# Optimization experiments

Measured on AMD Instinct MI355X. Metric: run time of the kernel, lower is better.

Reference implementation:

```python
import jax, jax.numpy as jnp
import numpy as np
from jax import lax

IMG = 28
K = 3
OUT = IMG - K + 1  # 26

def setup_inputs() -> dict:
    key = jax.random.key(0)
    k1, k2, k3 = jax.random.split(key, 3)
    B = 32768
    x = jax.random.normal(k1, (B, IMG * IMG), dtype=jnp.float32)
    conv_w = jax.random.normal(k2, (K, K), dtype=jnp.float32)
    W = jax.random.normal(k3, (IMG * IMG - 0, 1), dtype=jnp.float32)  # placeholder
    W = jax.random.normal(k3, (OUT * OUT, 10), dtype=jnp.float32) * 0.02
    b = jnp.zeros((10,), dtype=jnp.float32)
    return {"x": x, "conv_w": conv_w, "W": W, "b": b}

def reference(x, conv_w, W, b):
    B = x.shape[0]
    img = x.reshape(B, 1, IMG, IMG)            # NCHW
    ker = conv_w.reshape(1, 1, K, K)           # OIHW
    # The original Convolve is cross-correlation (slice * weight), which
    # matches lax.conv_general_dilated's default semantics.
    conv = lax.conv_general_dilated(
        img, ker, window_strides=(1, 1), padding='VALID',
        dimension_numbers=('NCHW', 'OIHW', 'NCHW'))  # [B,1,26,26]
    h = jax.nn.relu(conv.reshape(B, OUT * OUT))
    return h @ W + b
```

## Files before the change

kernel.cpp:

```cpp
#include <hip/hip_runtime.h>

#define IMGD 28
#define OUTD 26
#define NCLS 10
#define NIMG 64
#define UPB 29
#define BWORDS (NIMG * UPB * 4)
#define NBAND 7
#define THREADS 1024
#define LDSTRIDE 11

typedef float v2f __attribute__((ext_vector_type(2)));

__device__ __forceinline__ void gload_lds16(const float* gp, float* lp) {
    __builtin_amdgcn_global_load_lds(
        (const __attribute__((address_space(1))) void*)gp,
        (__attribute__((address_space(3))) void*)lp, 16, 0, 0);
}

__device__ __forceinline__ void stage_band(const float* __restrict__ x,
                                           int img_base, int B, int r0,
                                           float* buf, int wv, int lane)
{
#pragma unroll
    for (int it = 0; it < 2; ++it) {
        const int fw = it * 16 + wv;
        if (fw < UPB) {
            const int f = fw * 64 + lane;
            const int g = f / UPB;
            const int s = f - g * UPB;
            const int q = (s == 28) ? 27 : s;
            int gi = img_base + g; if (gi >= B) gi = B - 1;
            const float* gp = x + (size_t)gi * (IMGD * IMGD) + r0 * IMGD + q * 4;
            gload_lds16(gp, buf + fw * 256);
        }
    }
}

template<int NU>
__device__ __forceinline__ void read_row(const float* buf, int lane, int br, int u0,
                                         float* dst)
{
    const float4* b4 = (const float4*)buf;
#pragma unroll
    for (int u = 0; u < NU; ++u) {
        float4 a = b4[lane * UPB + br * 7 + u0 + u];
        dst[4*u+0] = a.x; dst[4*u+1] = a.y; dst[4*u+2] = a.z; dst[4*u+3] = a.w;
    }
}

template<int WID, int OFF>
__device__ __forceinline__ void conv_row(const float* X, const float* Y, const float* Z,
                                         const float (&kk)[9],
                                         const float* __restrict__ wr, v2f* acc)
{
#pragma unroll
    for (int c = 0; c < WID; ++c) {
        float p0 = fmaf(X[OFF+c], kk[0], X[OFF+c+1] * kk[1]);
        p0 = fmaf(X[OFF+c+2], kk[2], p0);
        float p1 = fmaf(Y[OFF+c], kk[3], Y[OFF+c+1] * kk[4]);
        p1 = fmaf(Y[OFF+c+2], kk[5], p1);
        float p2 = fmaf(Z[OFF+c], kk[6], Z[OFF+c+1] * kk[7]);
        p2 = fmaf(Z[OFF+c+2], kk[8], p2);
        float v = fmaxf((p0 + p1) + p2, 0.0f);
        const float* w = wr + c * NCLS;
#pragma unroll
        for (int p = 0; p < 5; ++p) {
            v2f wv2 = *(const v2f*)(w + 2 * p);
            v2f vv; vv[0] = v; vv[1] = v;
            acc[p] += vv * wv2;
        }
    }
}

template<int WID, int NU, int OFF>
__device__ __forceinline__ void run_all(
    const float* __restrict__ x, int img_base, int B,
    float* lds0, int wv, int lane, int rg, int u0, int c0,
    const float* __restrict__ cw, const float* __restrict__ Wp, v2f* acc)
{
    float kk[9];
#pragma unroll
    for (int i = 0; i < 9; ++i) kk[i] = cw[i];

    float S[2][4 * NU];

    stage_band(x, img_base, B, 0, lds0, wv, lane);

    for (int k = 0; k < NBAND; ++k) {
        asm volatile("s_waitcnt vmcnt(0)" ::: "memory");
        __builtin_amdgcn_s_barrier();

        if (k + 1 < NBAND)
            stage_band(x, img_base, B, 4 * (k + 1),
                       lds0 + ((k + 1) & 1) * BWORDS, wv, lane);

        const float* buf = lds0 + (k & 1) * BWORDS;

        if (rg == 0) {
            float R[4][4 * NU];
#pragma unroll
            for (int br = 0; br < 4; ++br) read_row<NU>(buf, lane, br, u0, R[br]);
            conv_row<WID, OFF>(R[0], R[1], R[2], kk,
                               Wp + ((size_t)(4 * k) * OUTD + c0) * NCLS, acc);
            conv_row<WID, OFF>(R[1], R[2], R[3], kk,
                               Wp + ((size_t)(4 * k + 1) * OUTD + c0) * NCLS, acc);
        } else {
            if (k > 0) {
                float T[2][4 * NU];
                read_row<NU>(buf, lane, 0, u0, T[0]);
                read_row<NU>(buf, lane, 1, u0, T[1]);
                conv_row<WID, OFF>(S[0], S[1], T[0], kk,
                                   Wp + ((size_t)(4 * k - 2) * OUTD + c0) * NCLS, acc);
                conv_row<WID, OFF>(S[1], T[0], T[1], kk,
                                   Wp + ((size_t)(4 * k - 1) * OUTD + c0) * NCLS, acc);
            }
            if (k < NBAND - 1) {
                read_row<NU>(buf, lane, 2, u0, S[0]);
                read_row<NU>(buf, lane, 3, u0, S[1]);
            }
        }
    }
}

__global__ __launch_bounds__(THREADS, 8) void fused_conv_relu_fc(
    const float* __restrict__ x,
    const float* __restrict__ cw,
    const float* __restrict__ Wp,
    const float* __restrict__ bp,
    float* __restrict__ out,
    int B)
{
    __shared__ float lds[2 * BWORDS];

    const int lane = threadIdx.x & 63;
    const int wv   = __builtin_amdgcn_readfirstlane((int)(threadIdx.x >> 6));
    const int rg   = wv >> 3;
    const int cs   = wv & 7;
    const int img_base = blockIdx.x * NIMG;

    v2f acc[5];
#pragma unroll
    for (int p = 0; p < 5; ++p) { acc[p][0] = 0.0f; acc[p][1] = 0.0f; }

    if      (cs < 5)  run_all<4,2,0>(x, img_base, B, lds, wv, lane, rg, cs, 4*cs, cw, Wp, acc);
    else if (cs == 5) run_all<2,1,0>(x, img_base, B, lds, wv, lane, rg, 5,  20,   cw, Wp, acc);
    else if (cs == 6) run_all<2,2,2>(x, img_base, B, lds, wv, lane, rg, 5,  22,   cw, Wp, acc);
    else              run_all<2,1,0>(x, img_base, B, lds, wv, lane, rg, 6,  24,   cw, Wp, acc);

    __syncthreads();

    float* part = lds;
    float* myp = &part[(wv * 64 + lane) * LDSTRIDE];
#pragma unroll
    for (int p = 0; p < 5; ++p) { myp[2*p] = acc[p][0]; myp[2*p+1] = acc[p][1]; }
    __syncthreads();

    const int o = threadIdx.x;
    if (o < NIMG * NCLS) {
        const int im = o / NCLS;
        const int c  = o - im * NCLS;
        float s = bp[c];
#pragma unroll
        for (int w2 = 0; w2 < 16; ++w2)
            s += part[(w2 * 64 + im) * LDSTRIDE + c];
        if (img_base + im < B)
            out[(size_t)(img_base + im) * NCLS + c] = s;
    }
}

extern "C" void kernel_launch(void* const* d_in, const int* in_sizes, int n_in,
                              void* d_out, int out_size, void* d_ws, size_t ws_size,
                              hipStream_t stream) {
    const float* x  = (const float*)d_in[0];
    const float* cw = (const float*)d_in[1];
    const float* Wp = (const float*)d_in[2];
    const float* bp = (const float*)d_in[3];
    float* out = (float*)d_out;

    const int B = in_sizes[0] / (IMGD * IMGD);
    const int grid = (B + NIMG - 1) / NIMG;

    fused_conv_relu_fc<<<grid, THREADS, 0, stream>>>(x, cw, Wp, bp, out, B);
}
```

Baseline: 34.33 us.

## Triple-buffer 3-row bands and split columns across 13 waves

Input rows are now staged in 3-row bands (21 float4 units, no padding unit) into a triple-buffered LDS ring, with two bands in flight and per-wave vmcnt waits instead of a full drain. Each of 13 waves handles 2 output columns across all rows, and 3 waves only help with staging. This replaces the old two-row-group split with its 4-row bands. The aim is to overlap global loads with compute more deeply and drop the redundant padding load. In exchange it leaves some waves idle during compute, copies rows between registers each band, and uses more LDS per block.

```diff
diff --git a/kernel.cpp b/kernel.cpp
--- a/kernel.cpp
+++ b/kernel.cpp
@@ -4,9 +4,9 @@
 #define OUTD 26
 #define NCLS 10
 #define NIMG 64
-#define UPB 29
-#define BWORDS (NIMG * UPB * 4)
-#define NBAND 7
+#define U3 21
+#define U1 7
+#define BW3 (NIMG * U3 * 4)
 #define THREADS 1024
 #define LDSTRIDE 11
 
@@ -18,44 +18,44 @@
         (__attribute__((address_space(3))) void*)lp, 16, 0, 0);
 }
 
+template<int UNITS>
 __device__ __forceinline__ void stage_band(const float* __restrict__ x,
                                            int img_base, int B, int r0,
                                            float* buf, int wv, int lane)
 {
 #pragma unroll
-    for (int it = 0; it < 2; ++it) {
+    for (int it = 0; it * 16 < UNITS; ++it) {
         const int fw = it * 16 + wv;
-        if (fw < UPB) {
+        if (fw < UNITS) {
             const int f = fw * 64 + lane;
-            const int g = f / UPB;
-            const int s = f - g * UPB;
-            const int q = (s == 28) ? 27 : s;
+            const int g = f / UNITS;
+            const int s = f - g * UNITS;
             int gi = img_base + g; if (gi >= B) gi = B - 1;
-            const float* gp = x + (size_t)gi * (IMGD * IMGD) + r0 * IMGD + q * 4;
+            const float* gp = x + (size_t)gi * (IMGD * IMGD) + r0 * IMGD + s * 4;
             gload_lds16(gp, buf + fw * 256);
         }
     }
 }
 
-template<int NU>
+template<int NU, int STRIDE>
 __device__ __forceinline__ void read_row(const float* buf, int lane, int br, int u0,
                                          float* dst)
 {
     const float4* b4 = (const float4*)buf;
 #pragma unroll
     for (int u = 0; u < NU; ++u) {
-        float4 a = b4[lane * UPB + br * 7 + u0 + u];
+        float4 a = b4[lane * STRIDE + br * 7 + u0 + u];
         dst[4*u+0] = a.x; dst[4*u+1] = a.y; dst[4*u+2] = a.z; dst[4*u+3] = a.w;
     }
 }
 
-template<int WID, int OFF>
-__device__ __forceinline__ void conv_row(const float* X, const float* Y, const float* Z,
-                                         const float (&kk)[9],
+template<int OFF, int NR>
+__device__ __forceinline__ void conv_row(const float (&X)[NR], const float (&Y)[NR],
+                                         const float (&Z)[NR], const float (&kk)[9],
                                          const float* __restrict__ wr, v2f* acc)
 {
 #pragma unroll
-    for (int c = 0; c < WID; ++c) {
+    for (int c = 0; c < 2; ++c) {
         float p0 = fmaf(X[OFF+c], kk[0], X[OFF+c+1] * kk[1]);
         p0 = fmaf(X[OFF+c+2], kk[2], p0);
         float p1 = fmaf(Y[OFF+c], kk[3], Y[OFF+c+1] * kk[4]);
@@ -73,53 +73,66 @@
     }
 }
 
-template<int WID, int NU, int OFF>
+template<int NU, int OFF>
 __device__ __forceinline__ void run_all(
     const float* __restrict__ x, int img_base, int B,
-    float* lds0, int wv, int lane, int rg, int u0, int c0,
+    float* lds0, int wv, int lane, int u0, int c0,
     const float* __restrict__ cw, const float* __restrict__ Wp, v2f* acc)
 {
+    constexpr int NR = 4 * (NU ? NU : 1);
     float kk[9];
 #pragma unroll
     for (int i = 0; i < 9; ++i) kk[i] = cw[i];
 
-    float S[2][4 * NU];
+    float S0[NR], S1[NR];
 
-    stage_band(x, img_base, B, 0, lds0, wv, lane);
+    stage_band<U3>(x, img_base, B, 0, lds0,       wv, lane);
+    stage_band<U3>(x, img_base, B, 3, lds0 + BW3, wv, lane);
 
-    for (int k = 0; k < NBAND; ++k) {
-        asm volatile("s_waitcnt vmcnt(0)" ::: "memory");
+#pragma unroll
+    for (int k = 0; k < 9; ++k) {
+        if (k < 8) {
+            if (wv < 5) asm volatile("s_waitcnt vmcnt(2)" ::: "memory");
+            else        asm volatile("s_waitcnt vmcnt(1)" ::: "memory");
+        } else {
+            if (wv < 7) asm volatile("s_waitcnt vmcnt(1)" ::: "memory");
+            else        asm volatile("s_waitcnt vmcnt(0)" ::: "memory");
+        }
         __builtin_amdgcn_s_barrier();
 
-        if (k + 1 < NBAND)
-            stage_band(x, img_base, B, 4 * (k + 1),
-                       lds0 + ((k + 1) & 1) * BWORDS, wv, lane);
+        if (k < 7)
+            stage_band<U3>(x, img_base, B, 3 * (k + 2),
+                           lds0 + ((k + 2) % 3) * BW3, wv, lane);
+        else if (k == 7)
+            stage_band<U1>(x, img_base, B, 27, lds0, wv, lane);
 
-        const float* buf = lds0 + (k & 1) * BWORDS;
+        const float* buf = lds0 + (k % 3) * BW3;
 
-        if (rg == 0) {
-            float R[4][4 * NU];
+        if (NU > 0) {
+            float Ta[NR], Tb[NR], Tc[NR];
+            read_row<(NU?NU:1), U3>(buf, lane, 0, u0, Ta);
+            if (k > 0)
+                conv_row<OFF>(S0, S1, Ta, kk,
+                              Wp + ((size_t)(3*k-2) * OUTD + c0) * NCLS, acc);
+            read_row<(NU?NU:1), U3>(buf, lane, 1, u0, Tb);
+            if (k > 0)
+                conv_row<OFF>(S1, Ta, Tb, kk,
+                              Wp + ((size_t)(3*k-1) * OUTD + c0) * NCLS, acc);
+            read_row<(NU?NU:1), U3>(buf, lane, 2, u0, Tc);
+            conv_row<OFF>(Ta, Tb, Tc, kk,
+                          Wp + ((size_t)(3*k) * OUTD + c0) * NCLS, acc);
 #pragma unroll
-            for (int br = 0; br < 4; ++br) read_row<NU>(buf, lane, br, u0, R[br]);
-            conv_row<WID, OFF>(R[0], R[1], R[2], kk,
-                               Wp + ((size_t)(4 * k) * OUTD + c0) * NCLS, acc);
-            conv_row<WID, OFF>(R[1], R[2], R[3], kk,
-                               Wp + ((size_t)(4 * k + 1) * OUTD + c0) * NCLS, acc);
-        } else {
-            if (k > 0) {
-                float T[2][4 * NU];
-                read_row<NU>(buf, lane, 0, u0, T[0]);
-                read_row<NU>(buf, lane, 1, u0, T[1]);
-                conv_row<WID, OFF>(S[0], S[1], T[0], kk,
-                                   Wp + ((size_t)(4 * k - 2) * OUTD + c0) * NCLS, acc);
-                conv_row<WID, OFF>(S[1], T[0], T[1], kk,
-                                   Wp + ((size_t)(4 * k - 1) * OUTD + c0) * NCLS, acc);
-            }
-            if (k < NBAND - 1) {
-                read_row<NU>(buf, lane, 2, u0, S[0]);
-                read_row<NU>(buf, lane, 3, u0, S[1]);
-            }
+            for (int i = 0; i < NR; ++i) { S0[i] = Tb[i]; S1[i] = Tc[i]; }
         }
+    }
+
+    asm volatile("s_waitcnt vmcnt(0)" ::: "memory");
+    __builtin_amdgcn_s_barrier();
+    if (NU > 0) {
+        float Ta[NR];
+        read_row<(NU?NU:1), U1>(lds0, lane, 0, u0, Ta);
+        conv_row<OFF>(S0, S1, Ta, kk,
+                      Wp + ((size_t)25 * OUTD + c0) * NCLS, acc);
     }
 }
 
@@ -131,22 +144,20 @@
     float* __restrict__ out,
     int B)
 {
-    __shared__ float lds[2 * BWORDS];
+    __shared__ float lds[3 * BW3];
 
     const int lane = threadIdx.x & 63;
     const int wv   = __builtin_amdgcn_readfirstlane((int)(threadIdx.x >> 6));
-    const int rg   = wv >> 3;
-    const int cs   = wv & 7;
     const int img_base = blockIdx.x * NIMG;
 
     v2f acc[5];
 #pragma unroll
     for (int p = 0; p < 5; ++p) { acc[p][0] = 0.0f; acc[p][1] = 0.0f; }
 
-    if      (cs < 5)  run_all<4,2,0>(x, img_base, B, lds, wv, lane, rg, cs, 4*cs, cw, Wp, acc);
-    else if (cs == 5) run_all<2,1,0>(x, img_base, B, lds, wv, lane, rg, 5,  20,   cw, Wp, acc);
-    else if (cs == 6) run_all<2,2,2>(x, img_base, B, lds, wv, lane, rg, 5,  22,   cw, Wp, acc);
-    else              run_all<2,1,0>(x, img_base, B, lds, wv, lane, rg, 6,  24,   cw, Wp, acc);
+    if (wv < 13) {
+        if (wv & 1) run_all<2,2>(x, img_base, B, lds, wv, lane, (wv-1)/2, 2*wv, cw, Wp, acc);
+        else        run_all<1,0>(x, img_base, B, lds, wv, lane, wv/2,     2*wv, cw, Wp, acc);
+    } else        run_all<0,0>(x, img_base, B, lds, wv, lane, 0, 0, cw, Wp, acc);
 
     __syncthreads();
 
```

Result: slower. 55.69 us (+62.2%).
